# Performance work log

Measured on AMD Instinct MI355X. Metric: run time of the kernel, lower is better.

Reference implementation:

```python
import jax, jax.numpy as jnp
import numpy as np

ALPHA = 0.5

def setup_inputs() -> dict:
    key = jax.random.key(0)
    k1, k2 = jax.random.split(key)
    B, S, F_IN, F_OUT = 64, 512, 1024, 1024
    x = jax.random.normal(k1, (B, S, F_IN), dtype=jnp.float32)
    W = jax.random.normal(k2, (F_OUT, F_IN), dtype=jnp.float32) * (F_IN ** -0.5)
    return {"x": x, "W": W}

def reference(x, W):
    # x: [B, S, F_in], W: [F_out, F_in] (torch Linear layout, no bias)
    alpha = jnp.asarray(ALPHA, dtype=x.dtype)
    # Project all segments at once (the big GEMM), then scan the EMA recurrence.
    y = jnp.einsum('bsf,of->bso', x, W)  # [B, S, F_out]
    y_t = jnp.swapaxes(y, 0, 1)          # [S, B, F_out] for scan over segments

    def step(h, yk):
        h = alpha * h + (1 - alpha) * yk
        return h, h

    h0 = jnp.zeros((x.shape[0], W.shape[0]), dtype=x.dtype)
    hk, hiddens_t = jax.lax.scan(step, h0, y_t)
    hiddens = jnp.swapaxes(hiddens_t, 0, 1)  # [B, S, F_out]
    return (hk, hiddens)
```

## Files before the change

### kernel.cpp

```cpp
#include <hip/hip_runtime.h>
#include <hip/hip_bf16.h>
#include <stdint.h>

#define B_DIM 64
#define S_DIM 512
#define K_DIM 1024
#define N_DIM 1024
#define M_DIM (B_DIM * S_DIM)

typedef __attribute__((ext_vector_type(8))) short short8;
typedef __attribute__((ext_vector_type(4))) float floatx4;

__global__ __launch_bounds__(256) void scan_x_kernel(
    const float* __restrict__ x, __hip_bfloat16* __restrict__ xs) {
  int t = blockIdx.x * 256 + threadIdx.x;
  int b = t >> 10;
  int f = t & 1023;
  const float* px = x + (size_t)b * S_DIM * K_DIM + f;
  __hip_bfloat16* ps = xs + (size_t)b * S_DIM * K_DIM + f;
  float h = 0.0f;
  #pragma unroll 16
  for (int s = 0; s < S_DIM; ++s) {
    float v = px[(size_t)s * K_DIM];
    h = 0.5f * (h + v);
    ps[(size_t)s * K_DIM] = __float2bfloat16(h);
  }
}

__global__ __launch_bounds__(256) void conv_w_kernel(
    const float* __restrict__ W, __hip_bfloat16* __restrict__ Wb) {
  int t = blockIdx.x * 256 + threadIdx.x;
  Wb[t] = __float2bfloat16(W[t]);
}

__global__ __launch_bounds__(256) void gemm_kernel(
    const __hip_bfloat16* __restrict__ A,
    const __hip_bfloat16* __restrict__ Bw,
    float* __restrict__ out) {
  __shared__ __hip_bfloat16 lA[128 * 32];
  __shared__ __hip_bfloat16 lB[128 * 32];

  const int tid  = threadIdx.x;
  const int lane = tid & 63;
  const int w    = tid >> 6;
  const int wm   = (w >> 1) * 64;
  const int wn   = (w & 1) * 64;
  const int quad = lane >> 4;
  const int l15  = lane & 15;

  const int n0 = blockIdx.x * 128;
  const int m0 = blockIdx.y * 128;

  floatx4 acc[4][4] = {};

  for (int k0 = 0; k0 < K_DIM; k0 += 32) {
    #pragma unroll
    for (int p = 0; p < 2; ++p) {
      int c  = tid + p * 256;
      int r  = c >> 2;
      int kc = (c & 3) * 8;
      const __hip_bfloat16* ga = A  + (size_t)(m0 + r) * K_DIM + k0 + kc;
      const __hip_bfloat16* gb = Bw + (size_t)(n0 + r) * K_DIM + k0 + kc;
      __builtin_amdgcn_global_load_lds(
          (const __attribute__((address_space(1))) void*)ga,
          (__attribute__((address_space(3))) void*)&lA[c * 8], 16, 0, 0);
      __builtin_amdgcn_global_load_lds(
          (const __attribute__((address_space(1))) void*)gb,
          (__attribute__((address_space(3))) void*)&lB[c * 8], 16, 0, 0);
    }
    __syncthreads();

    short8 af[4], bfr[4];
    #pragma unroll
    for (int i = 0; i < 4; ++i) {
      af[i]  = *(const short8*)&lA[(wm + i * 16 + l15) * 32 + quad * 8];
      bfr[i] = *(const short8*)&lB[(wn + i * 16 + l15) * 32 + quad * 8];
    }
    #pragma unroll
    for (int i = 0; i < 4; ++i)
      #pragma unroll
      for (int j = 0; j < 4; ++j)
        acc[i][j] = __builtin_amdgcn_mfma_f32_16x16x32_bf16(
            af[i], bfr[j], acc[i][j], 0, 0, 0);
    __syncthreads();
  }

  float* hid = out + B_DIM * N_DIM;
  #pragma unroll
  for (int i = 0; i < 4; ++i) {
    #pragma unroll
    for (int j = 0; j < 4; ++j) {
      #pragma unroll
      for (int r = 0; r < 4; ++r) {
        int gm = m0 + wm + i * 16 + quad * 4 + r;
        int gn = n0 + wn + j * 16 + l15;
        float v = acc[i][j][r];
        hid[(size_t)gm * N_DIM + gn] = v;
        if ((gm & (S_DIM - 1)) == (S_DIM - 1)) {
          out[(size_t)(gm >> 9) * N_DIM + gn] = v;
        }
      }
    }
  }
}

extern "C" void kernel_launch(void* const* d_in, const int* in_sizes, int n_in,
                              void* d_out, int out_size, void* d_ws, size_t ws_size,
                              hipStream_t stream) {
  const float* x = (const float*)d_in[0];
  const float* W = (const float*)d_in[1];
  float* out = (float*)d_out;

  __hip_bfloat16* xs = (__hip_bfloat16*)d_ws;
  __hip_bfloat16* Wb = (__hip_bfloat16*)((char*)d_ws + (size_t)M_DIM * K_DIM * 2);

  scan_x_kernel<<<dim3((B_DIM * K_DIM) / 256), dim3(256), 0, stream>>>(x, xs);
  conv_w_kernel<<<dim3((N_DIM * K_DIM) / 256), dim3(256), 0, stream>>>(W, Wb);
  gemm_kernel<<<dim3(N_DIM / 128, M_DIM / 128), dim3(256), 0, stream>>>(xs, Wb, out);
}
```

Before: 342.6 us.

## Chunk EMA scan over sequence with truncated warmup and swizzle GEMM LDS layout

The scan kernel now splits the sequence into 8 chunks of 64 steps per thread and processes four features at once with float4 loads and packed bf16 stores. Each chunk warms up over the previous 32 steps instead of the full prefix, relying on the 0.5 decay making earlier contributions negligible. The goal is more parallelism in the memory-bound prefilter, at the cost of redundant reads and an approximation. The GEMM also XOR-swizzles its LDS tile placement to reduce bank conflicts on fragment reads.

```diff
diff --git a/kernel.cpp b/kernel.cpp
--- a/kernel.cpp
+++ b/kernel.cpp
@@ -13,17 +13,35 @@
 
 __global__ __launch_bounds__(256) void scan_x_kernel(
     const float* __restrict__ x, __hip_bfloat16* __restrict__ xs) {
-  int t = blockIdx.x * 256 + threadIdx.x;
-  int b = t >> 10;
-  int f = t & 1023;
-  const float* px = x + (size_t)b * S_DIM * K_DIM + f;
-  __hip_bfloat16* ps = xs + (size_t)b * S_DIM * K_DIM + f;
-  float h = 0.0f;
-  #pragma unroll 16
-  for (int s = 0; s < S_DIM; ++s) {
-    float v = px[(size_t)s * K_DIM];
-    h = 0.5f * (h + v);
-    ps[(size_t)s * K_DIM] = __float2bfloat16(h);
+  const int t  = blockIdx.x * 256 + threadIdx.x;
+  const int f4 = (t & 255) << 2;
+  const int c  = (t >> 8) & 7;
+  const int b  = t >> 11;
+  const size_t base = (size_t)b * S_DIM * K_DIM + f4;
+  const int s0 = c * 64;
+
+  float4 h = {0.f, 0.f, 0.f, 0.f};
+  if (c != 0) {
+    #pragma unroll 8
+    for (int s = s0 - 32; s < s0; ++s) {
+      float4 v = *(const float4*)(x + base + (size_t)s * K_DIM);
+      h.x = 0.5f * (h.x + v.x); h.y = 0.5f * (h.y + v.y);
+      h.z = 0.5f * (h.z + v.z); h.w = 0.5f * (h.w + v.w);
+    }
+  }
+  #pragma unroll 8
+  for (int s = s0; s < s0 + 64; ++s) {
+    float4 v = *(const float4*)(x + base + (size_t)s * K_DIM);
+    h.x = 0.5f * (h.x + v.x); h.y = 0.5f * (h.y + v.y);
+    h.z = 0.5f * (h.z + v.z); h.w = 0.5f * (h.w + v.w);
+    __hip_bfloat16 b0 = __float2bfloat16(h.x);
+    __hip_bfloat16 b1 = __float2bfloat16(h.y);
+    __hip_bfloat16 b2 = __float2bfloat16(h.z);
+    __hip_bfloat16 b3 = __float2bfloat16(h.w);
+    union { unsigned short u[4]; uint2 v2; } pk;
+    pk.u[0] = *(unsigned short*)&b0; pk.u[1] = *(unsigned short*)&b1;
+    pk.u[2] = *(unsigned short*)&b2; pk.u[3] = *(unsigned short*)&b3;
+    *(uint2*)(xs + base + (size_t)s * K_DIM) = pk.v2;
   }
 }
 
@@ -47,6 +65,7 @@
   const int wn   = (w & 1) * 64;
   const int quad = lane >> 4;
   const int l15  = lane & 15;
+  const int sw   = ((quad ^ ((l15 >> 1) & 3)) * 8);
 
   const int n0 = blockIdx.x * 128;
   const int m0 = blockIdx.y * 128;
@@ -56,9 +75,10 @@
   for (int k0 = 0; k0 < K_DIM; k0 += 32) {
     #pragma unroll
     for (int p = 0; p < 2; ++p) {
-      int c  = tid + p * 256;
-      int r  = c >> 2;
-      int kc = (c & 3) * 8;
+      int c    = tid + p * 256;
+      int r    = c >> 2;
+      int slot = c & 3;
+      int kc   = (slot ^ ((r >> 1) & 3)) * 8;
       const __hip_bfloat16* ga = A  + (size_t)(m0 + r) * K_DIM + k0 + kc;
       const __hip_bfloat16* gb = Bw + (size_t)(n0 + r) * K_DIM + k0 + kc;
       __builtin_amdgcn_global_load_lds(
@@ -73,8 +93,8 @@
     short8 af[4], bfr[4];
     #pragma unroll
     for (int i = 0; i < 4; ++i) {
-      af[i]  = *(const short8*)&lA[(wm + i * 16 + l15) * 32 + quad * 8];
-      bfr[i] = *(const short8*)&lB[(wn + i * 16 + l15) * 32 + quad * 8];
+      af[i]  = *(const short8*)&lA[(wm + i * 16 + l15) * 32 + sw];
+      bfr[i] = *(const short8*)&lB[(wn + i * 16 + l15) * 32 + sw];
     }
     #pragma unroll
     for (int i = 0; i < 4; ++i)
@@ -114,7 +134,7 @@
   __hip_bfloat16* xs = (__hip_bfloat16*)d_ws;
   __hip_bfloat16* Wb = (__hip_bfloat16*)((char*)d_ws + (size_t)M_DIM * K_DIM * 2);
 
-  scan_x_kernel<<<dim3((B_DIM * K_DIM) / 256), dim3(256), 0, stream>>>(x, xs);
+  scan_x_kernel<<<dim3(131072 / 256), dim3(256), 0, stream>>>(x, xs);
   conv_w_kernel<<<dim3((N_DIM * K_DIM) / 256), dim3(256), 0, stream>>>(W, Wb);
   gemm_kernel<<<dim3(N_DIM / 128, M_DIM / 128), dim3(256), 0, stream>>>(xs, Wb, out);
 }
```

After: 343.9 us. About the same (+0.4%).
